# Performance work log

Hardware: AMD Instinct MI355X
Metric: run time of the kernel (lower is better)

Reference implementation:

```python
import jax, jax.numpy as jnp
import numpy as np

N_IN, N_OUT, H = 32, 31, 128
B1, B2 = 256, 256


def setup_inputs() -> dict:
    key = jax.random.key(0)
    ks = jax.random.split(key, 6)
    def lin(k, o, i):
        return jax.random.normal(k, (o, i), jnp.float32) / np.float32(np.sqrt(i))
    return {
        "t": jax.random.uniform(ks[0], (), jnp.float32),
        "y": jax.random.normal(ks[1], (B1, B2, N_OUT), jnp.float32),
        "W0": lin(ks[2], H, N_IN), "b0": jnp.zeros((H,), jnp.float32),
        "W1": lin(ks[3], H, H),    "b1": jnp.zeros((H,), jnp.float32),
        "W2": lin(ks[4], H, H),    "b2": jnp.zeros((H,), jnp.float32),
        "W3": lin(ks[5], N_OUT, H), "b3": jnp.zeros((N_OUT,), jnp.float32),
    }


def reference(t, y, W0, b0, W1, b1, W2, b2, W3, b3):
    # inp[..., :-1] = y ; inp[..., -1] = force(t) with force = sin
    force = jnp.sin(t)
    inp = jnp.concatenate(
        [y, jnp.broadcast_to(force, y.shape[:-1] + (1,))], axis=-1
    )  # [B1, B2, N_IN]

    def model(x):  # x: [N_IN]
        h = jnp.tanh(W0 @ x + b0)
        h = jnp.tanh(W1 @ h + b1)
        h = jnp.tanh(W2 @ h + b2)
        return W3 @ h + b3  # [N_OUT]

    out = jax.vmap(jax.vmap(model))(inp)  # [B1, B2, N_OUT]
    # vmap(vmap(jacrev(model)))(inp)[..., :-1] -> drop d/d(force) column
    jac = jax.vmap(jax.vmap(jax.jacrev(model)))(inp)[..., :-1]  # [B1,B2,N_OUT,N_IN-1]
    return out, jac
```

## Files before the change

### kernel.cpp

```cpp
#include <hip/hip_runtime.h>
#include <hip/hip_bf16.h>
#include <math.h>


using short8 = __attribute__((ext_vector_type(8))) short;
using f32x4  = __attribute__((ext_vector_type(4))) float;

#define PB 4
#define PPB 32
#define STRIDE 136

__device__ __forceinline__ float fast_tanh(float z) {
    float e = __expf(2.0f * z);
    return 1.0f - 2.0f * __builtin_amdgcn_rcpf(e + 1.0f);
}

__device__ __forceinline__ unsigned pk2(float lo, float hi) {
    unsigned r;
    asm("v_cvt_pk_bf16_f32 %0, %1, %2" : "=v"(r) : "v"(lo), "v"(hi));
    return r;
}

__device__ __forceinline__ ushort f2bf1(float f) {
    union { float f; unsigned u; } v; v.f = f;
    unsigned r = v.u + 0x7fffu + ((v.u >> 16) & 1u);
    return (ushort)(r >> 16);
}

__device__ __forceinline__ short8 pack8f(const float* s) {
    union { unsigned u[4]; short8 v; } r;
    #pragma unroll
    for (int q = 0; q < 4; ++q) r.u[q] = pk2(s[2 * q], s[2 * q + 1]);
    return r.v;
}

__global__ void __launch_bounds__(512, 4)
node_mfma(const float* __restrict__ tptr,
          const float* __restrict__ y,
          const float* __restrict__ W0, const float* __restrict__ b0,
          const float* __restrict__ W1, const float* __restrict__ b1,
          const float* __restrict__ W2, const float* __restrict__ b2,
          const float* __restrict__ W3, const float* __restrict__ b3,
          float* __restrict__ out, float* __restrict__ jac, int npts) {
    __shared__ __align__(16) ushort XT[2][PB][32][STRIDE];
    __shared__ float xb[PB][32];

    const int tid  = threadIdx.x;
    const int w    = tid >> 6;
    const int lane = tid & 63;
    const int r16  = lane & 15;
    const int g    = lane >> 4;
    const int j    = 16 * w + r16;

    float w0f[8];
    {
        const float4* p4 = reinterpret_cast<const float4*>(W0 + j * 32 + g * 8);
        float4 q0 = p4[0], q1 = p4[1];
        w0f[0]=q0.x; w0f[1]=q0.y; w0f[2]=q0.z; w0f[3]=q0.w;
        w0f[4]=q1.x; w0f[5]=q1.y; w0f[6]=q1.z; w0f[7]=q1.w;
    }
    short8 aW[2][4];
    #pragma unroll
    for (int L = 0; L < 2; ++L) {
        const float* WL = L ? W2 : W1;
        #pragma unroll
        for (int kc = 0; kc < 4; ++kc) {
            float tmp[8];
            const float4* p4 = reinterpret_cast<const float4*>(WL + j * 128 + kc * 32 + g * 8);
            float4 q0 = p4[0], q1 = p4[1];
            tmp[0]=q0.x; tmp[1]=q0.y; tmp[2]=q0.z; tmp[3]=q0.w;
            tmp[4]=q1.x; tmp[5]=q1.y; tmp[6]=q1.z; tmp[7]=q1.w;
            aW[L][kc] = pack8f(tmp);
        }
    }
    const int mw = (w >> 1) & 1, nw = w & 1;
    const int r3 = 16 * mw + r16;
    short8 aW3[4];
    #pragma unroll
    for (int kc = 0; kc < 4; ++kc) {
        float tmp[8];
        if (r3 < 31) {
            const float4* p4 = reinterpret_cast<const float4*>(W3 + r3 * 128 + kc * 32 + g * 8);
            float4 q0 = p4[0], q1 = p4[1];
            tmp[0]=q0.x; tmp[1]=q0.y; tmp[2]=q0.z; tmp[3]=q0.w;
            tmp[4]=q1.x; tmp[5]=q1.y; tmp[6]=q1.z; tmp[7]=q1.w;
        } else {
            #pragma unroll
            for (int i = 0; i < 8; ++i) tmp[i] = 0.0f;
        }
        aW3[kc] = pack8f(tmp);
    }
    const float b0v = b0[j];
    float bv[2][4], b3v[4];
    #pragma unroll
    for (int reg = 0; reg < 4; ++reg) {
        bv[0][reg] = b1[16 * w + 4 * g + reg];
        bv[1][reg] = b2[16 * w + 4 * g + reg];
        int o = 16 * mw + 4 * g + reg;
        b3v[reg] = (o < 31) ? b3[o] : 0.0f;
    }
    const float force = sinf(tptr[0]);

    const int pl0 = tid >> 5, c0 = tid & 31;
    const bool act = tid < PB * 32;
    float pf = 0.0f;
    if (act && c0 < 31) pf = y[(size_t)(blockIdx.x * PPB + pl0) * 31 + c0];

    for (int pass = 0; pass < PPB / PB; ++pass) {
        const int pbase = blockIdx.x * PPB + pass * PB;

        if (act) xb[pl0][c0] = (c0 < 31) ? pf : force;
        __syncthreads();

        #pragma unroll
        for (int pl = 0; pl < PB; ++pl) {
            float zp = 0.0f;
            #pragma unroll
            for (int i = 0; i < 8; ++i) zp = fmaf(w0f[i], xb[pl][g * 8 + i], zp);
            zp += __shfl_xor(zp, 16, 64);
            zp += __shfl_xor(zp, 32, 64);
            float h = fast_tanh(zp + b0v);
            float d = 1.0f - h * h;
            #pragma unroll
            for (int i = 0; i < 8; ++i) {
                int c = g * 8 + i;
                XT[0][pl][c][j] = f2bf1((c == 31) ? h : d * w0f[i]);
            }
        }

        if (act && c0 < 31 && pass + 1 < PPB / PB)
            pf = y[(size_t)(pbase + PB + pl0) * 31 + c0];

        __syncthreads();

        #pragma unroll
        for (int L = 0; L < 2; ++L) {
            #pragma unroll
            for (int pl = 0; pl < PB; ++pl) {
                f32x4 a0 = {0.f, 0.f, 0.f, 0.f}, a1 = {0.f, 0.f, 0.f, 0.f};
                __builtin_amdgcn_s_setprio(1);
                #pragma unroll
                for (int kc = 0; kc < 4; ++kc) {
                    short8 bf0 = *reinterpret_cast<const short8*>(&XT[L][pl][r16][kc * 32 + g * 8]);
                    short8 bf1 = *reinterpret_cast<const short8*>(&XT[L][pl][16 + r16][kc * 32 + g * 8]);
                    a0 = __builtin_amdgcn_mfma_f32_16x16x32_bf16(aW[L][kc], bf0, a0, 0, 0, 0);
                    a1 = __builtin_amdgcn_mfma_f32_16x16x32_bf16(aW[L][kc], bf1, a1, 0, 0, 0);
                }
                __builtin_amdgcn_s_setprio(0);
                float va[4], vb[4];
                #pragma unroll
                for (int reg = 0; reg < 4; ++reg) {
                    float tv = fast_tanh(a1[reg] + bv[L][reg]);
                    float d  = 1.0f - tv * tv;
                    float dd = __shfl(d, lane | 15, 64);
                    va[reg] = dd * a0[reg];
                    vb[reg] = (r16 == 15) ? tv : dd * a1[reg];
                }
                uint2 pa, pb;
                pa.x = pk2(va[0], va[1]); pa.y = pk2(va[2], va[3]);
                pb.x = pk2(vb[0], vb[1]); pb.y = pk2(vb[2], vb[3]);
                *reinterpret_cast<uint2*>(&XT[1 - L][pl][r16][16 * w + 4 * g])      = pa;
                *reinterpret_cast<uint2*>(&XT[1 - L][pl][16 + r16][16 * w + 4 * g]) = pb;
            }
            __syncthreads();
        }

        #pragma unroll
        for (int tsk = 0; tsk < 2; ++tsk) {
            int pl = (w >> 2) + tsk * 2;
            f32x4 a = {0.f, 0.f, 0.f, 0.f};
            __builtin_amdgcn_s_setprio(1);
            #pragma unroll
            for (int kc = 0; kc < 4; ++kc) {
                short8 bf = *reinterpret_cast<const short8*>(&XT[0][pl][16 * nw + r16][kc * 32 + g * 8]);
                a = __builtin_amdgcn_mfma_f32_16x16x32_bf16(aW3[kc], bf, a, 0, 0, 0);
            }
            __builtin_amdgcn_s_setprio(0);
            size_t p = (size_t)(pbase + pl);
            int c = 16 * nw + r16;
            if ((int)p < npts) {
                #pragma unroll
                for (int reg = 0; reg < 4; ++reg) {
                    int o = 16 * mw + 4 * g + reg;
                    if (o < 31) {
                        if (c == 31) out[p * 31 + o] = a[reg] + b3v[reg];
                        else         jac[(p * 31 + o) * 31 + c] = a[reg];
                    }
                }
            }
        }
    }
}

extern "C" void kernel_launch(void* const* d_in, const int* in_sizes, int n_in,
                              void* d_out, int out_size, void* d_ws, size_t ws_size,
                              hipStream_t stream) {
    const float* t  = (const float*)d_in[0];
    const float* y  = (const float*)d_in[1];
    const float* W0 = (const float*)d_in[2];
    const float* b0 = (const float*)d_in[3];
    const float* W1 = (const float*)d_in[4];
    const float* b1 = (const float*)d_in[5];
    const float* W2 = (const float*)d_in[6];
    const float* b2 = (const float*)d_in[7];
    const float* W3 = (const float*)d_in[8];
    const float* b3 = (const float*)d_in[9];

    const int npts = in_sizes[1] / 31;
    float* out = (float*)d_out;
    float* jac = out + (size_t)npts * 31;

    const int blocks = (npts + PPB - 1) / PPB;
    node_mfma<<<blocks, 512, 0, stream>>>(t, y, W0, b0, W1, b1, W2, b2, W3, b3,
                                          out, jac, npts);
}
```

Measured before the change: 322.4 us.

## Move layer-0 Jacobian seeding onto MFMA with identity input tiles, halve block size

Layer 0 now runs as an MFMA. Each point's input becomes a bf16 32x32 tile holding an identity block plus the input vector, so one matrix multiply yields both the pre-activation and the seed Jacobian, replacing the scalar FMA-and-shuffle path. Blocks shrink to 256 threads (4 waves). Each wave now covers two 64-row tiles of every hidden layer, and blocks process 2 points per pass over 16 points. Biases are stored in bf16 in LDS, which adds rounding error on the biases and raises register use from holding more weight fragments per wave.

```diff
diff --git a/kernel.cpp b/kernel.cpp
--- a/kernel.cpp
+++ b/kernel.cpp
@@ -6,189 +6,207 @@
 using short8 = __attribute__((ext_vector_type(8))) short;
 using f32x4  = __attribute__((ext_vector_type(4))) float;
 
-#define PB 4
-#define PPB 32
-#define STRIDE 136
+#define PB 2
+#define PPB 16
+#define NP (PPB / PB)
+#define ST 136
+#define SIN 40
 
 __device__ __forceinline__ float fast_tanh(float z) {
     float e = __expf(2.0f * z);
     return 1.0f - 2.0f * __builtin_amdgcn_rcpf(e + 1.0f);
 }
-
 __device__ __forceinline__ unsigned pk2(float lo, float hi) {
     unsigned r;
     asm("v_cvt_pk_bf16_f32 %0, %1, %2" : "=v"(r) : "v"(lo), "v"(hi));
     return r;
 }
-
+__device__ __forceinline__ float bf2f(ushort u) {
+    union { unsigned u; float f; } c; c.u = ((unsigned)u) << 16; return c.f;
+}
 __device__ __forceinline__ ushort f2bf1(float f) {
     union { float f; unsigned u; } v; v.f = f;
     unsigned r = v.u + 0x7fffu + ((v.u >> 16) & 1u);
     return (ushort)(r >> 16);
 }
-
 __device__ __forceinline__ short8 pack8f(const float* s) {
     union { unsigned u[4]; short8 v; } r;
     #pragma unroll
-    for (int q = 0; q < 4; ++q) r.u[q] = pk2(s[2 * q], s[2 * q + 1]);
+    for (int qq = 0; qq < 4; ++qq) r.u[qq] = pk2(s[2 * qq], s[2 * qq + 1]);
     return r.v;
 }
-
-__global__ void __launch_bounds__(512, 4)
-node_mfma(const float* __restrict__ tptr,
-          const float* __restrict__ y,
-          const float* __restrict__ W0, const float* __restrict__ b0,
-          const float* __restrict__ W1, const float* __restrict__ b1,
-          const float* __restrict__ W2, const float* __restrict__ b2,
-          const float* __restrict__ W3, const float* __restrict__ b3,
-          float* __restrict__ out, float* __restrict__ jac, int npts) {
-    __shared__ __align__(16) ushort XT[2][PB][32][STRIDE];
-    __shared__ float xb[PB][32];
+__device__ __forceinline__ short8 load_row8(const float* p) {
+    float tmp[8];
+    const float4* p4 = reinterpret_cast<const float4*>(p);
+    float4 q0 = p4[0], q1 = p4[1];
+    tmp[0]=q0.x; tmp[1]=q0.y; tmp[2]=q0.z; tmp[3]=q0.w;
+    tmp[4]=q1.x; tmp[5]=q1.y; tmp[6]=q1.z; tmp[7]=q1.w;
+    return pack8f(tmp);
+}
+
+__global__ void __launch_bounds__(256, 4)
+node_mfma2(const float* __restrict__ tptr,
+           const float* __restrict__ y,
+           const float* __restrict__ W0, const float* __restrict__ b0,
+           const float* __restrict__ W1, const float* __restrict__ b1,
+           const float* __restrict__ W2, const float* __restrict__ b2,
+           const float* __restrict__ W3, const float* __restrict__ b3,
+           float* __restrict__ out, float* __restrict__ jac, int npts) {
+    __shared__ __align__(16) ushort XT[2][PB][32][ST];
+    __shared__ __align__(16) ushort Xin[PB][32][SIN];
+    __shared__ __align__(16) ushort bbf[3][128];
+    __shared__ __align__(16) ushort b3bf[32];
 
     const int tid  = threadIdx.x;
     const int w    = tid >> 6;
     const int lane = tid & 63;
     const int r16  = lane & 15;
     const int g    = lane >> 4;
-    const int j    = 16 * w + r16;
-
-    float w0f[8];
-    {
-        const float4* p4 = reinterpret_cast<const float4*>(W0 + j * 32 + g * 8);
-        float4 q0 = p4[0], q1 = p4[1];
-        w0f[0]=q0.x; w0f[1]=q0.y; w0f[2]=q0.z; w0f[3]=q0.w;
-        w0f[4]=q1.x; w0f[5]=q1.y; w0f[6]=q1.z; w0f[7]=q1.w;
-    }
-    short8 aW[2][4];
+    const int q    = w;
+
+    short8 aW0[2];
+    short8 aW[2][2][4];
     #pragma unroll
-    for (int L = 0; L < 2; ++L) {
-        const float* WL = L ? W2 : W1;
+    for (int mt = 0; mt < 2; ++mt) {
+        const int row = 16 * q + 64 * mt + r16;
+        aW0[mt] = load_row8(W0 + row * 32 + g * 8);
         #pragma unroll
         for (int kc = 0; kc < 4; ++kc) {
-            float tmp[8];
-            const float4* p4 = reinterpret_cast<const float4*>(WL + j * 128 + kc * 32 + g * 8);
-            float4 q0 = p4[0], q1 = p4[1];
-            tmp[0]=q0.x; tmp[1]=q0.y; tmp[2]=q0.z; tmp[3]=q0.w;
-            tmp[4]=q1.x; tmp[5]=q1.y; tmp[6]=q1.z; tmp[7]=q1.w;
-            aW[L][kc] = pack8f(tmp);
-        }
-    }
-    const int mw = (w >> 1) & 1, nw = w & 1;
-    const int r3 = 16 * mw + r16;
+            aW[0][mt][kc] = load_row8(W1 + row * 128 + kc * 32 + g * 8);
+            aW[1][mt][kc] = load_row8(W2 + row * 128 + kc * 32 + g * 8);
+        }
+    }
+    const int pt3 = w >> 1, mt3 = w & 1;
+    const int r3 = 16 * mt3 + r16;
     short8 aW3[4];
     #pragma unroll
     for (int kc = 0; kc < 4; ++kc) {
-        float tmp[8];
-        if (r3 < 31) {
-            const float4* p4 = reinterpret_cast<const float4*>(W3 + r3 * 128 + kc * 32 + g * 8);
-            float4 q0 = p4[0], q1 = p4[1];
-            tmp[0]=q0.x; tmp[1]=q0.y; tmp[2]=q0.z; tmp[3]=q0.w;
-            tmp[4]=q1.x; tmp[5]=q1.y; tmp[6]=q1.z; tmp[7]=q1.w;
-        } else {
-            #pragma unroll
-            for (int i = 0; i < 8; ++i) tmp[i] = 0.0f;
-        }
-        aW3[kc] = pack8f(tmp);
-    }
-    const float b0v = b0[j];
-    float bv[2][4], b3v[4];
-    #pragma unroll
-    for (int reg = 0; reg < 4; ++reg) {
-        bv[0][reg] = b1[16 * w + 4 * g + reg];
-        bv[1][reg] = b2[16 * w + 4 * g + reg];
-        int o = 16 * mw + 4 * g + reg;
-        b3v[reg] = (o < 31) ? b3[o] : 0.0f;
-    }
+        if (r3 < 31) aW3[kc] = load_row8(W3 + r3 * 128 + kc * 32 + g * 8);
+        else { short8 z = {0,0,0,0,0,0,0,0}; aW3[kc] = z; }
+    }
+
+    for (int e = tid; e < 384; e += 256) {
+        int L = e >> 7, i = e & 127;
+        const float* bp = (L == 0) ? b0 : (L == 1) ? b1 : b2;
+        bbf[L][i] = f2bf1(bp[i]);
+    }
+    if (tid < 32) b3bf[tid] = (tid < 31) ? f2bf1(b3[tid]) : (ushort)0;
+    {
+        uint* xz = reinterpret_cast<uint*>(&Xin[0][0][0]);
+        for (int e = tid; e < PB * 32 * SIN / 2; e += 256) xz[e] = 0;
+    }
+    __syncthreads();
+    if (tid < PB * 31) {
+        int pt = tid / 31, c = tid % 31;
+        Xin[pt][c][c] = 0x3F80;
+    }
+
     const float force = sinf(tptr[0]);
 
+    const bool act = tid < PB * 32;
     const int pl0 = tid >> 5, c0 = tid & 31;
-    const bool act = tid < PB * 32;
     float pf = 0.0f;
     if (act && c0 < 31) pf = y[(size_t)(blockIdx.x * PPB + pl0) * 31 + c0];
-
-    for (int pass = 0; pass < PPB / PB; ++pass) {
+    if (act) Xin[pl0][31][c0] = f2bf1(c0 < 31 ? pf : force);
+    __syncthreads();
+
+    auto epi = [&](f32x4 a0, f32x4 a1, int mt, const ushort* bL, ushort* dst) {
+        const int row0 = 16 * q + 64 * mt;
+        uint2 bq = *reinterpret_cast<const uint2*>(&bL[row0 + 4 * g]);
+        const ushort* bqs = reinterpret_cast<const ushort*>(&bq);
+        float va[4], vb[4];
+        #pragma unroll
+        for (int reg = 0; reg < 4; ++reg) {
+            float tv = fast_tanh(a1[reg] + bf2f(bqs[reg]));
+            float d  = 1.0f - tv * tv;
+            float dd = __shfl(d, lane | 15, 64);
+            va[reg] = dd * a0[reg];
+            vb[reg] = (r16 == 15) ? tv : dd * a1[reg];
+        }
+        uint2 pa, pb;
+        pa.x = pk2(va[0], va[1]); pa.y = pk2(va[2], va[3]);
+        pb.x = pk2(vb[0], vb[1]); pb.y = pk2(vb[2], vb[3]);
+        *reinterpret_cast<uint2*>(&dst[r16 * ST + row0 + 4 * g])        = pa;
+        *reinterpret_cast<uint2*>(&dst[(16 + r16) * ST + row0 + 4 * g]) = pb;
+    };
+
+    for (int pass = 0; pass < NP; ++pass) {
         const int pbase = blockIdx.x * PPB + pass * PB;
 
-        if (act) xb[pl0][c0] = (c0 < 31) ? pf : force;
-        __syncthreads();
-
-        #pragma unroll
-        for (int pl = 0; pl < PB; ++pl) {
-            float zp = 0.0f;
-            #pragma unroll
-            for (int i = 0; i < 8; ++i) zp = fmaf(w0f[i], xb[pl][g * 8 + i], zp);
-            zp += __shfl_xor(zp, 16, 64);
-            zp += __shfl_xor(zp, 32, 64);
-            float h = fast_tanh(zp + b0v);
-            float d = 1.0f - h * h;
-            #pragma unroll
-            for (int i = 0; i < 8; ++i) {
-                int c = g * 8 + i;
-                XT[0][pl][c][j] = f2bf1((c == 31) ? h : d * w0f[i]);
-            }
-        }
-
-        if (act && c0 < 31 && pass + 1 < PPB / PB)
+        if (act && c0 < 31 && pass + 1 < NP)
             pf = y[(size_t)(pbase + PB + pl0) * 31 + c0];
 
+        #pragma unroll
+        for (int pt = 0; pt < PB; ++pt) {
+            const ushort* src = &Xin[pt][0][0];
+            short8 bf0 = *reinterpret_cast<const short8*>(&src[r16 * SIN + g * 8]);
+            short8 bf1 = *reinterpret_cast<const short8*>(&src[(16 + r16) * SIN + g * 8]);
+            f32x4 a00 = {0.f,0.f,0.f,0.f}, a01 = {0.f,0.f,0.f,0.f};
+            f32x4 a10 = {0.f,0.f,0.f,0.f}, a11 = {0.f,0.f,0.f,0.f};
+            __builtin_amdgcn_s_setprio(1);
+            a00 = __builtin_amdgcn_mfma_f32_16x16x32_bf16(aW0[0], bf0, a00, 0, 0, 0);
+            a01 = __builtin_amdgcn_mfma_f32_16x16x32_bf16(aW0[0], bf1, a01, 0, 0, 0);
+            a10 = __builtin_amdgcn_mfma_f32_16x16x32_bf16(aW0[1], bf0, a10, 0, 0, 0);
+            a11 = __builtin_amdgcn_mfma_f32_16x16x32_bf16(aW0[1], bf1, a11, 0, 0, 0);
+            __builtin_amdgcn_s_setprio(0);
+            epi(a00, a01, 0, bbf[0], &XT[0][pt][0][0]);
+            epi(a10, a11, 1, bbf[0], &XT[0][pt][0][0]);
+        }
         __syncthreads();
 
         #pragma unroll
         for (int L = 0; L < 2; ++L) {
             #pragma unroll
-            for (int pl = 0; pl < PB; ++pl) {
-                f32x4 a0 = {0.f, 0.f, 0.f, 0.f}, a1 = {0.f, 0.f, 0.f, 0.f};
+            for (int pt = 0; pt < PB; ++pt) {
+                f32x4 acc[2][2] = {{{0.f,0.f,0.f,0.f},{0.f,0.f,0.f,0.f}},
+                                   {{0.f,0.f,0.f,0.f},{0.f,0.f,0.f,0.f}}};
+                const ushort* src = &XT[L][pt][0][0];
                 __builtin_amdgcn_s_setprio(1);
                 #pragma unroll
                 for (int kc = 0; kc < 4; ++kc) {
-                    short8 bf0 = *reinterpret_cast<const short8*>(&XT[L][pl][r16][kc * 32 + g * 8]);
-                    short8 bf1 = *reinterpret_cast<const short8*>(&XT[L][pl][16 + r16][kc * 32 + g * 8]);
-                    a0 = __builtin_amdgcn_mfma_f32_16x16x32_bf16(aW[L][kc], bf0, a0, 0, 0, 0);
-                    a1 = __builtin_amdgcn_mfma_f32_16x16x32_bf16(aW[L][kc], bf1, a1, 0, 0, 0);
+                    short8 bf0 = *reinterpret_cast<const short8*>(&src[r16 * ST + kc * 32 + g * 8]);
+                    short8 bf1 = *reinterpret_cast<const short8*>(&src[(16 + r16) * ST + kc * 32 + g * 8]);
+                    acc[0][0] = __builtin_amdgcn_mfma_f32_16x16x32_bf16(aW[L][0][kc], bf0, acc[0][0], 0, 0, 0);
+                    acc[0][1] = __builtin_amdgcn_mfma_f32_16x16x32_bf16(aW[L][0][kc], bf1, acc[0][1], 0, 0, 0);
+                    acc[1][0] = __builtin_amdgcn_mfma_f32_16x16x32_bf16(aW[L][1][kc], bf0, acc[1][0], 0, 0, 0);
+                    acc[1][1] = __builtin_amdgcn_mfma_f32_16x16x32_bf16(aW[L][1][kc], bf1, acc[1][1], 0, 0, 0);
                 }
                 __builtin_amdgcn_s_setprio(0);
-                float va[4], vb[4];
-                #pragma unroll
-                for (int reg = 0; reg < 4; ++reg) {
-                    float tv = fast_tanh(a1[reg] + bv[L][reg]);
-                    float d  = 1.0f - tv * tv;
-                    float dd = __shfl(d, lane | 15, 64);
-                    va[reg] = dd * a0[reg];
-                    vb[reg] = (r16 == 15) ? tv : dd * a1[reg];
-                }
-                uint2 pa, pb;
-                pa.x = pk2(va[0], va[1]); pa.y = pk2(va[2], va[3]);
-                pb.x = pk2(vb[0], vb[1]); pb.y = pk2(vb[2], vb[3]);
-                *reinterpret_cast<uint2*>(&XT[1 - L][pl][r16][16 * w + 4 * g])      = pa;
-                *reinterpret_cast<uint2*>(&XT[1 - L][pl][16 + r16][16 * w + 4 * g]) = pb;
+                ushort* dst = &XT[1 - L][pt][0][0];
+                epi(acc[0][0], acc[0][1], 0, bbf[L + 1], dst);
+                epi(acc[1][0], acc[1][1], 1, bbf[L + 1], dst);
             }
             __syncthreads();
-        }
-
-        #pragma unroll
-        for (int tsk = 0; tsk < 2; ++tsk) {
-            int pl = (w >> 2) + tsk * 2;
-            f32x4 a = {0.f, 0.f, 0.f, 0.f};
+            if (L == 0 && act)
+                Xin[pl0][31][c0] = f2bf1(c0 < 31 ? pf : force);
+        }
+
+        {
+            const ushort* src = &XT[0][pt3][0][0];
+            f32x4 ca = {0.f,0.f,0.f,0.f}, cb = {0.f,0.f,0.f,0.f};
             __builtin_amdgcn_s_setprio(1);
             #pragma unroll
             for (int kc = 0; kc < 4; ++kc) {
-                short8 bf = *reinterpret_cast<const short8*>(&XT[0][pl][16 * nw + r16][kc * 32 + g * 8]);
-                a = __builtin_amdgcn_mfma_f32_16x16x32_bf16(aW3[kc], bf, a, 0, 0, 0);
+                short8 bf0 = *reinterpret_cast<const short8*>(&src[r16 * ST + kc * 32 + g * 8]);
+                short8 bf1 = *reinterpret_cast<const short8*>(&src[(16 + r16) * ST + kc * 32 + g * 8]);
+                ca = __builtin_amdgcn_mfma_f32_16x16x32_bf16(aW3[kc], bf0, ca, 0, 0, 0);
+                cb = __builtin_amdgcn_mfma_f32_16x16x32_bf16(aW3[kc], bf1, cb, 0, 0, 0);
             }
             __builtin_amdgcn_s_setprio(0);
-            size_t p = (size_t)(pbase + pl);
-            int c = 16 * nw + r16;
+            const size_t p = (size_t)(pbase + pt3);
             if ((int)p < npts) {
                 #pragma unroll
                 for (int reg = 0; reg < 4; ++reg) {
-                    int o = 16 * mw + 4 * g + reg;
+                    const int o = 16 * mt3 + 4 * g + reg;
                     if (o < 31) {
-                        if (c == 31) out[p * 31 + o] = a[reg] + b3v[reg];
-                        else         jac[(p * 31 + o) * 31 + c] = a[reg];
+                        jac[(p * 31 + o) * 31 + r16] = ca[reg];
+                        if (r16 < 15)       jac[(p * 31 + o) * 31 + 16 + r16] = cb[reg];
+                        else if (r16 == 15) out[p * 31 + o] = cb[reg] + bf2f(b3bf[o]);
                     }
                 }
             }
         }
+        __syncthreads();
     }
 }
 
@@ -211,6 +229,6 @@
     float* jac = out + (size_t)npts * 31;
 
     const int blocks = (npts + PPB - 1) / PPB;
-    node_mfma<<<blocks, 512, 0, stream>>>(t, y, W0, b0, W1, b1, W2, b2, W3, b3,
-                                          out, jac, npts);
-}
+    node_mfma2<<<blocks, 256, 0, stream>>>(t, y, W0, b0, W1, b1, W2, b2, W3, b3,
+                                           out, jac, npts);
+}
```

Result: slower. 404.4 us (+25.4%).

## Split hidden-layer MFMA work by point groups with two row tiles per wave

Applied to the files above, without the earlier changes.

Each wave now computes two 16-row tiles of W1/W2 output (rows q*16 and q*16+64) for only two of the four points, instead of one row tile for all four points. The B-operand LDS reads per wave drop by half, since each loaded XT fragment feeds two MFMAs instead of one. The cost is double the weight registers (aW grows to 2x2x4 short8), which may raise VGPR pressure and hurt occupancy under the 512x4 launch bound.

```diff
diff --git a/kernel.cpp b/kernel.cpp
--- a/kernel.cpp
+++ b/kernel.cpp
@@ -30,8 +30,17 @@
 __device__ __forceinline__ short8 pack8f(const float* s) {
     union { unsigned u[4]; short8 v; } r;
     #pragma unroll
-    for (int q = 0; q < 4; ++q) r.u[q] = pk2(s[2 * q], s[2 * q + 1]);
+    for (int qq = 0; qq < 4; ++qq) r.u[qq] = pk2(s[2 * qq], s[2 * qq + 1]);
     return r.v;
+}
+
+__device__ __forceinline__ short8 load_row8(const float* p) {
+    float tmp[8];
+    const float4* p4 = reinterpret_cast<const float4*>(p);
+    float4 q0 = p4[0], q1 = p4[1];
+    tmp[0]=q0.x; tmp[1]=q0.y; tmp[2]=q0.z; tmp[3]=q0.w;
+    tmp[4]=q1.x; tmp[5]=q1.y; tmp[6]=q1.z; tmp[7]=q1.w;
+    return pack8f(tmp);
 }
 
 __global__ void __launch_bounds__(512, 4)
@@ -51,6 +60,8 @@
     const int r16  = lane & 15;
     const int g    = lane >> 4;
     const int j    = 16 * w + r16;
+    const int q    = w & 3;
+    const int pg   = w >> 2;
 
     float w0f[8];
     {
@@ -59,18 +70,14 @@
         w0f[0]=q0.x; w0f[1]=q0.y; w0f[2]=q0.z; w0f[3]=q0.w;
         w0f[4]=q1.x; w0f[5]=q1.y; w0f[6]=q1.z; w0f[7]=q1.w;
     }
-    short8 aW[2][4];
-    #pragma unroll
-    for (int L = 0; L < 2; ++L) {
-        const float* WL = L ? W2 : W1;
+    short8 aW[2][2][4];
+    #pragma unroll
+    for (int mt = 0; mt < 2; ++mt) {
+        const int row = 16 * q + 64 * mt + r16;
         #pragma unroll
         for (int kc = 0; kc < 4; ++kc) {
-            float tmp[8];
-            const float4* p4 = reinterpret_cast<const float4*>(WL + j * 128 + kc * 32 + g * 8);
-            float4 q0 = p4[0], q1 = p4[1];
-            tmp[0]=q0.x; tmp[1]=q0.y; tmp[2]=q0.z; tmp[3]=q0.w;
-            tmp[4]=q1.x; tmp[5]=q1.y; tmp[6]=q1.z; tmp[7]=q1.w;
-            aW[L][kc] = pack8f(tmp);
+            aW[0][mt][kc] = load_row8(W1 + row * 128 + kc * 32 + g * 8);
+            aW[1][mt][kc] = load_row8(W2 + row * 128 + kc * 32 + g * 8);
         }
     }
     const int mw = (w >> 1) & 1, nw = w & 1;
@@ -78,24 +85,18 @@
     short8 aW3[4];
     #pragma unroll
     for (int kc = 0; kc < 4; ++kc) {
-        float tmp[8];
-        if (r3 < 31) {
-            const float4* p4 = reinterpret_cast<const float4*>(W3 + r3 * 128 + kc * 32 + g * 8);
-            float4 q0 = p4[0], q1 = p4[1];
-            tmp[0]=q0.x; tmp[1]=q0.y; tmp[2]=q0.z; tmp[3]=q0.w;
-            tmp[4]=q1.x; tmp[5]=q1.y; tmp[6]=q1.z; tmp[7]=q1.w;
-        } else {
-            #pragma unroll
-            for (int i = 0; i < 8; ++i) tmp[i] = 0.0f;
-        }
-        aW3[kc] = pack8f(tmp);
+        if (r3 < 31) aW3[kc] = load_row8(W3 + r3 * 128 + kc * 32 + g * 8);
+        else { short8 z = {0,0,0,0,0,0,0,0}; aW3[kc] = z; }
     }
     const float b0v = b0[j];
-    float bv[2][4], b3v[4];
+    float bv[2][2][4], b3v[4];
     #pragma unroll
     for (int reg = 0; reg < 4; ++reg) {
-        bv[0][reg] = b1[16 * w + 4 * g + reg];
-        bv[1][reg] = b2[16 * w + 4 * g + reg];
+        #pragma unroll
+        for (int mt = 0; mt < 2; ++mt) {
+            bv[0][mt][reg] = b1[16 * q + 64 * mt + 4 * g + reg];
+            bv[1][mt][reg] = b2[16 * q + 64 * mt + 4 * g + reg];
+        }
         int o = 16 * mw + 4 * g + reg;
         b3v[reg] = (o < 31) ? b3[o] : 0.0f;
     }
@@ -136,31 +137,39 @@
         #pragma unroll
         for (int L = 0; L < 2; ++L) {
             #pragma unroll
-            for (int pl = 0; pl < PB; ++pl) {
-                f32x4 a0 = {0.f, 0.f, 0.f, 0.f}, a1 = {0.f, 0.f, 0.f, 0.f};
+            for (int pi = 0; pi < 2; ++pi) {
+                const int pl = 2 * pg + pi;
+                f32x4 acc[2][2] = {{{0.f,0.f,0.f,0.f},{0.f,0.f,0.f,0.f}},
+                                   {{0.f,0.f,0.f,0.f},{0.f,0.f,0.f,0.f}}};
                 __builtin_amdgcn_s_setprio(1);
                 #pragma unroll
                 for (int kc = 0; kc < 4; ++kc) {
                     short8 bf0 = *reinterpret_cast<const short8*>(&XT[L][pl][r16][kc * 32 + g * 8]);
                     short8 bf1 = *reinterpret_cast<const short8*>(&XT[L][pl][16 + r16][kc * 32 + g * 8]);
-                    a0 = __builtin_amdgcn_mfma_f32_16x16x32_bf16(aW[L][kc], bf0, a0, 0, 0, 0);
-                    a1 = __builtin_amdgcn_mfma_f32_16x16x32_bf16(aW[L][kc], bf1, a1, 0, 0, 0);
+                    acc[0][0] = __builtin_amdgcn_mfma_f32_16x16x32_bf16(aW[L][0][kc], bf0, acc[0][0], 0, 0, 0);
+                    acc[0][1] = __builtin_amdgcn_mfma_f32_16x16x32_bf16(aW[L][0][kc], bf1, acc[0][1], 0, 0, 0);
+                    acc[1][0] = __builtin_amdgcn_mfma_f32_16x16x32_bf16(aW[L][1][kc], bf0, acc[1][0], 0, 0, 0);
+                    acc[1][1] = __builtin_amdgcn_mfma_f32_16x16x32_bf16(aW[L][1][kc], bf1, acc[1][1], 0, 0, 0);
                 }
                 __builtin_amdgcn_s_setprio(0);
-                float va[4], vb[4];
                 #pragma unroll
-                for (int reg = 0; reg < 4; ++reg) {
-                    float tv = fast_tanh(a1[reg] + bv[L][reg]);
-                    float d  = 1.0f - tv * tv;
-                    float dd = __shfl(d, lane | 15, 64);
-                    va[reg] = dd * a0[reg];
-                    vb[reg] = (r16 == 15) ? tv : dd * a1[reg];
+                for (int mt = 0; mt < 2; ++mt) {
+                    float va[4], vb[4];
+                    #pragma unroll
+                    for (int reg = 0; reg < 4; ++reg) {
+                        float tv = fast_tanh(acc[mt][1][reg] + bv[L][mt][reg]);
+                        float d  = 1.0f - tv * tv;
+                        float dd = __shfl(d, lane | 15, 64);
+                        va[reg] = dd * acc[mt][0][reg];
+                        vb[reg] = (r16 == 15) ? tv : dd * acc[mt][1][reg];
+                    }
+                    uint2 pa, pb;
+                    pa.x = pk2(va[0], va[1]); pa.y = pk2(va[2], va[3]);
+                    pb.x = pk2(vb[0], vb[1]); pb.y = pk2(vb[2], vb[3]);
+                    const int col = 16 * q + 64 * mt + 4 * g;
+                    *reinterpret_cast<uint2*>(&XT[1 - L][pl][r16][col])      = pa;
+                    *reinterpret_cast<uint2*>(&XT[1 - L][pl][16 + r16][col]) = pb;
                 }
-                uint2 pa, pb;
-                pa.x = pk2(va[0], va[1]); pa.y = pk2(va[2], va[3]);
-                pb.x = pk2(vb[0], vb[1]); pb.y = pk2(vb[2], vb[3]);
-                *reinterpret_cast<uint2*>(&XT[1 - L][pl][r16][16 * w + 4 * g])      = pa;
-                *reinterpret_cast<uint2*>(&XT[1 - L][pl][16 + r16][16 * w + 4 * g]) = pb;
             }
             __syncthreads();
         }
```

Result: slower. 527.5 us (+63.6%).
